# Performance work log

Hardware: AMD Instinct MI355X
Metric: run time of the kernel (lower is better)

Reference implementation:

```python
import jax, jax.numpy as jnp
import numpy as np

B, L, D, H, DH, FF = 4, 1024, 1024, 16, 64, 4096
EPS = 1e-5


def _layer_norm(x, g, b):
    m = jnp.mean(x, -1, keepdims=True)
    v = jnp.mean((x - m) ** 2, -1, keepdims=True)
    return (x - m) * jax.lax.rsqrt(v + EPS) * g + b


def setup_inputs() -> dict:
    key = jax.random.key(0)
    ks = jax.random.split(key, 20)
    s = 0.02  # param init scale
    return {
        "x": jax.random.normal(ks[0], (B, L, D), jnp.float32),
        "adj_mask_matrix": jax.random.uniform(ks[1], (B * H, L, L), jnp.float32),
        "com_mask_matrix": jax.random.uniform(ks[2], (B * H, L, L), jnp.float32),
        "lattice_rel": jax.random.normal(ks[3], (2, 1, 1, DH), jnp.float32),
        "Wq": jax.random.normal(ks[4], (D, D), jnp.float32) * s,
        "bq": jnp.zeros((D,), jnp.float32),
        "Wk": jax.random.normal(ks[5], (D, D), jnp.float32) * s,
        "bk": jnp.zeros((D,), jnp.float32),
        "Wv": jax.random.normal(ks[6], (D, D), jnp.float32) * s,
        "bv": jnp.zeros((D,), jnp.float32),
        "Wo": jax.random.normal(ks[7], (D, D), jnp.float32) * s,
        "bo": jnp.zeros((D,), jnp.float32),
        "ln1_scale": jnp.ones((D,), jnp.float32),
        "ln1_bias": jnp.zeros((D,), jnp.float32),
        "W1": jax.random.normal(ks[8], (D, FF), jnp.float32) * s,
        "b1": jnp.zeros((FF,), jnp.float32),
        "W2": jax.random.normal(ks[9], (FF, D), jnp.float32) * s,
        "b2": jnp.zeros((D,), jnp.float32),
        "ln2_scale": jnp.ones((D,), jnp.float32),
        "ln2_bias": jnp.zeros((D,), jnp.float32),
    }


def reference(x, adj_mask_matrix, com_mask_matrix, lattice_rel,
              Wq, bq, Wk, bk, Wv, bv, Wo, bo, ln1_scale, ln1_bias,
              W1, b1, W2, b2, ln2_scale, ln2_bias):
    Bsz, Ln, Dm = x.shape
    # QKV projections; flat reshape [B,L,H*dh] -> [B*H,L,dh] matches torch .view
    Q = (x @ Wq + bq).reshape(Bsz * H, Ln, DH)
    K = (x @ Wk + bk).reshape(Bsz * H, Ln, DH)
    V = (x @ Wv + bv).reshape(Bsz * H, Ln, DH)
    scale = DH ** (-0.5)
    adj_rel = lattice_rel[0]  # [1,1,dh] broadcasts over (B*H, L)
    com_rel = lattice_rel[1]
    att_adj = jnp.einsum('bqd,bkd->bqk', Q + adj_rel, K + adj_rel) * scale
    att_com = jnp.einsum('bqd,bkd->bqk', Q + com_rel, K + com_rel) * scale
    # post-softmax multiplicative masking, then sum of the two attention maps
    mask_att = (jax.nn.softmax(att_adj, axis=-1) * adj_mask_matrix
                + jax.nn.softmax(att_com, axis=-1) * com_mask_matrix)
    context = jnp.matmul(mask_att, V).reshape(Bsz, Ln, H * DH)
    out = _layer_norm(context @ Wo + bo + x, ln1_scale, ln1_bias)
    ff = jax.nn.relu(out @ W1 + b1) @ W2 + b2
    return _layer_norm(ff + out, ln2_scale, ln2_bias)
```

## Files before the change

kernel.cpp:

```cpp
#include <hip/hip_runtime.h>
#include <hip/hip_bf16.h>

typedef __attribute__((ext_vector_type(8))) short s16x8;
typedef __attribute__((ext_vector_type(4))) float f32x4;
typedef unsigned short u16;
typedef unsigned int u32;

__device__ __forceinline__ u16 f2b(float f) {
    u32 u = __float_as_uint(f);
    u32 r = (u + 0x7fffu + ((u >> 16) & 1u)) >> 16;
    return (u16)r;
}
__device__ __forceinline__ float b2f(u16 b) {
    return __uint_as_float(((u32)b) << 16);
}

#define MFMA16(a, b, c) __builtin_amdgcn_mfma_f32_16x16x32_bf16(a, b, c, 0, 0, 0)
#define GLDS(gp, lp)                                                              \
    __builtin_amdgcn_global_load_lds((const __attribute__((address_space(1))) void*)(gp), \
                                     (__attribute__((address_space(3))) void*)(lp), 16, 0, 0)

__global__ void k_f2b(const float* __restrict__ in, u16* __restrict__ out, int n4) {
    int i = blockIdx.x * 256 + threadIdx.x;
    if (i >= n4) return;
    float4 v = ((const float4*)in)[i];
    ushort4 o;
    o.x = f2b(v.x); o.y = f2b(v.y); o.z = f2b(v.z); o.w = f2b(v.w);
    ((ushort4*)out)[i] = o;
}

__global__ void k_wtrans(const float* __restrict__ W, u16* __restrict__ Wt, int K, int N) {
    __shared__ float t[32][33];
    int bx = blockIdx.x * 32, by = blockIdx.y * 32;
    int tx = threadIdx.x, ty = threadIdx.y;
    for (int i = 0; i < 32; i += 8)
        t[ty + i][tx] = W[(size_t)(by + ty + i) * N + bx + tx];
    __syncthreads();
    for (int i = 0; i < 32; i += 8)
        Wt[(size_t)(bx + ty + i) * K + by + tx] = f2b(t[tx][ty + i]);
}

__global__ __launch_bounds__(256) void gemm_qkv(const u16* __restrict__ A, const u16* __restrict__ Bt,
                                                const float* __restrict__ bq, const float* __restrict__ bk,
                                                const float* __restrict__ bv,
                                                u16* __restrict__ Qb, u16* __restrict__ Kb,
                                                u16* __restrict__ Vt) {
    __shared__ __align__(16) short lA[128 * 64];
    __shared__ __align__(16) short lB[128 * 64];
    const int tid = threadIdx.x, lane = tid & 63, w = tid >> 6;
    const int l15 = lane & 15, lg = lane >> 4;
    const int wr = w >> 1, wc = w & 1;
    const int m0 = blockIdx.y * 128, n0 = blockIdx.x * 128;
    const int KK = 1024;
    f32x4 acc[4][4] = {};

    for (int k0 = 0; k0 < KK; k0 += 64) {
        #pragma unroll
        for (int i = 0; i < 4; i++) {
            int chunk = w * 4 + i;
            int arow = m0 + chunk * 8 + (lane >> 3);
            GLDS(A + (size_t)arow * KK + k0 + (lane & 7) * 8, (short*)lA + chunk * 512);
            int brow = n0 + chunk * 8 + (lane >> 3);
            GLDS(Bt + (size_t)brow * KK + k0 + (lane & 7) * 8, (short*)lB + chunk * 512);
        }
        __syncthreads();
        #pragma unroll
        for (int ks = 0; ks < 2; ks++) {
            s16x8 af[4], bfr[4];
            #pragma unroll
            for (int m = 0; m < 4; m++)
                af[m] = *(const s16x8*)&lA[(wr * 64 + m * 16 + l15) * 64 + ks * 32 + lg * 8];
            #pragma unroll
            for (int n = 0; n < 4; n++)
                bfr[n] = *(const s16x8*)&lB[(wc * 64 + n * 16 + l15) * 64 + ks * 32 + lg * 8];
            #pragma unroll
            for (int m = 0; m < 4; m++)
                #pragma unroll
                for (int n = 0; n < 4; n++)
                    acc[m][n] = MFMA16(af[m], bfr[n], acc[m][n]);
        }
        __syncthreads();
    }
    const int rbase = m0 + wr * 64, cbase = n0 + wc * 64;
    const int seg = cbase >> 10;
    #pragma unroll
    for (int m = 0; m < 4; m++)
        #pragma unroll
        for (int n = 0; n < 4; n++) {
            int col = cbase + n * 16 + l15;
            int c1 = col & 1023, d = col & 63;
            int row0 = rbase + m * 16 + lg * 4;
            if (seg == 0) {
                float bb = bq[c1];
                #pragma unroll
                for (int r = 0; r < 4; r++)
                    Qb[(size_t)(row0 + r) * 1024 + c1] = f2b(acc[m][n][r] + bb);
            } else if (seg == 1) {
                float bb = bk[c1];
                #pragma unroll
                for (int r = 0; r < 4; r++)
                    Kb[(size_t)(row0 + r) * 1024 + c1] = f2b(acc[m][n][r] + bb);
            } else {
                float bb = bv[c1];
                #pragma unroll
                for (int r = 0; r < 4; r++) {
                    int row = row0 + r;
                    size_t o = (size_t)(row >> 6) * 65536 + (size_t)d * 1024 + (row & 63) * 16 + (c1 >> 6);
                    Vt[o] = f2b(acc[m][n][r] + bb);
                }
            }
        }
}

template <int EPI>
__global__ __launch_bounds__(256) void gemm_bt(const u16* __restrict__ A, const u16* __restrict__ Bt,
                                               void* __restrict__ Cv, int M, int N, int K,
                                               const float* __restrict__ bias) {
    __shared__ __align__(16) short lA[128 * 64];
    __shared__ __align__(16) short lB[128 * 64];
    const int tid = threadIdx.x, lane = tid & 63, w = tid >> 6;
    const int l15 = lane & 15, lg = lane >> 4;
    const int wr = w >> 1, wc = w & 1;
    const int m0 = blockIdx.y * 128, n0 = blockIdx.x * 128;
    f32x4 acc[4][4] = {};

    for (int k0 = 0; k0 < K; k0 += 64) {
        #pragma unroll
        for (int i = 0; i < 4; i++) {
            int chunk = w * 4 + i;
            int arow = m0 + chunk * 8 + (lane >> 3);
            GLDS(A + (size_t)arow * K + k0 + (lane & 7) * 8, (short*)lA + chunk * 512);
            int brow = n0 + chunk * 8 + (lane >> 3);
            GLDS(Bt + (size_t)brow * K + k0 + (lane & 7) * 8, (short*)lB + chunk * 512);
        }
        __syncthreads();
        #pragma unroll
        for (int ks = 0; ks < 2; ks++) {
            s16x8 af[4], bfr[4];
            #pragma unroll
            for (int m = 0; m < 4; m++)
                af[m] = *(const s16x8*)&lA[(wr * 64 + m * 16 + l15) * 64 + ks * 32 + lg * 8];
            #pragma unroll
            for (int n = 0; n < 4; n++)
                bfr[n] = *(const s16x8*)&lB[(wc * 64 + n * 16 + l15) * 64 + ks * 32 + lg * 8];
            #pragma unroll
            for (int m = 0; m < 4; m++)
                #pragma unroll
                for (int n = 0; n < 4; n++)
                    acc[m][n] = MFMA16(af[m], bfr[n], acc[m][n]);
        }
        __syncthreads();
    }
    const int rbase = m0 + wr * 64, cbase = n0 + wc * 64;
    #pragma unroll
    for (int m = 0; m < 4; m++)
        #pragma unroll
        for (int n = 0; n < 4; n++) {
            int col = cbase + n * 16 + l15;
            int row0 = rbase + m * 16 + lg * 4;
            u16* C = (u16*)Cv;
            float bv = bias[col];
            #pragma unroll
            for (int r = 0; r < 4; r++)
                C[(size_t)(row0 + r) * N + col] = f2b(fmaxf(acc[m][n][r] + bv, 0.f));
        }
}

__global__ __launch_bounds__(256) void gemm_bt64(const u16* __restrict__ A, const u16* __restrict__ Bt,
                                                 float* __restrict__ C, int M, int N, int K) {
    __shared__ __align__(16) short lA[128 * 64];
    __shared__ __align__(16) short lB[64 * 64];
    const int tid = threadIdx.x, lane = tid & 63, w = tid >> 6;
    const int l15 = lane & 15, lg = lane >> 4;
    const int m0 = blockIdx.y * 128, n0 = blockIdx.x * 64;
    f32x4 acc[2][4] = {};

    for (int k0 = 0; k0 < K; k0 += 64) {
        #pragma unroll
        for (int i = 0; i < 4; i++) {
            int chunk = w * 4 + i;
            int arow = m0 + chunk * 8 + (lane >> 3);
            GLDS(A + (size_t)arow * K + k0 + (lane & 7) * 8, (short*)lA + chunk * 512);
        }
        #pragma unroll
        for (int i = 0; i < 2; i++) {
            int chunk = w * 2 + i;
            int brow = n0 + chunk * 8 + (lane >> 3);
            GLDS(Bt + (size_t)brow * K + k0 + (lane & 7) * 8, (short*)lB + chunk * 512);
        }
        __syncthreads();
        #pragma unroll
        for (int ks = 0; ks < 2; ks++) {
            s16x8 af[2], bfr[4];
            #pragma unroll
            for (int m = 0; m < 2; m++)
                af[m] = *(const s16x8*)&lA[(w * 32 + m * 16 + l15) * 64 + ks * 32 + lg * 8];
            #pragma unroll
            for (int n = 0; n < 4; n++)
                bfr[n] = *(const s16x8*)&lB[(n * 16 + l15) * 64 + ks * 32 + lg * 8];
            #pragma unroll
            for (int m = 0; m < 2; m++)
                #pragma unroll
                for (int n = 0; n < 4; n++)
                    acc[m][n] = MFMA16(af[m], bfr[n], acc[m][n]);
        }
        __syncthreads();
    }
    #pragma unroll
    for (int m = 0; m < 2; m++)
        #pragma unroll
        for (int n = 0; n < 4; n++) {
            int col = n0 + n * 16 + l15;
            int row0 = m0 + w * 32 + m * 16 + lg * 4;
            #pragma unroll
            for (int r = 0; r < 4; r++)
                C[(size_t)(row0 + r) * N + col] = acc[m][n][r];
        }
}

__global__ void k_fvec(const u16* __restrict__ Kb, const float* __restrict__ rel,
                       float* __restrict__ fa, float* __restrict__ fc) {
    __shared__ float rs[128];
    const int g = blockIdx.x, tid = threadIdx.x;
    if (tid < 128) rs[tid] = rel[tid];
    __syncthreads();
    for (int k = tid; k < 1024; k += 256) {
        const u16* kr = Kb + (size_t)g * 65536 + (size_t)k * 64;
        float sa = 0.f, sc = 0.f;
        #pragma unroll
        for (int j = 0; j < 8; j++) {
            s16x8 v = *(const s16x8*)(kr + j * 8);
            #pragma unroll
            for (int e = 0; e < 8; e++) {
                float kv = b2f((u16)v[e]);
                sa += kv * rs[j * 8 + e];
                sc += kv * rs[64 + j * 8 + e];
            }
        }
        fa[g * 1024 + k] = __expf(sa * 0.125f);
        fc[g * 1024 + k] = __expf(sc * 0.125f);
    }
}

__global__ __launch_bounds__(256, 2) void k_qke0(const u16* __restrict__ Qb, const u16* __restrict__ Kb,
                                                 const float* __restrict__ fa, const float* __restrict__ fc,
                                                 u16* __restrict__ E0,
                                                 float* __restrict__ la_, float* __restrict__ lc_) {
    const int bid = blockIdx.x;
    const int xcd = bid & 7, j = bid >> 3;
    const int g = xcd * 8 + (j & 7), qt = j >> 3;
    const int tid = threadIdx.x, lane = tid & 63, w = tid >> 6;
    const int l15 = lane & 15, lg = lane >> 4;
    __shared__ __align__(16) float lE[4][16][68];

    const int q0 = qt * 64 + w * 16;
    const size_t gQ = (size_t)g * 65536;
    const float scale = 0.125f;

    s16x8 qf[2];
    #pragma unroll
    for (int ks = 0; ks < 2; ks++)
        qf[ks] = *(const s16x8*)(Qb + gQ + (size_t)(q0 + l15) * 64 + ks * 32 + lg * 8);

    float la[4] = {0.f, 0.f, 0.f, 0.f}, lc[4] = {0.f, 0.f, 0.f, 0.f};
    const int srow = lane >> 2, sjj = lane & 3;

    #pragma unroll 1
    for (int it = 0; it < 16; it++) {
        const int kb = it * 64;
        f32x4 sa[4] = {};
        s16x8 kf[8];
        #pragma unroll
        for (int ks = 0; ks < 2; ks++)
            #pragma unroll
            for (int n = 0; n < 4; n++)
                kf[ks * 4 + n] = *(const s16x8*)(Kb + gQ + (size_t)(kb + n * 16 + l15) * 64 + ks * 32 + lg * 8);
        #pragma unroll
        for (int ks = 0; ks < 2; ks++)
            #pragma unroll
            for (int n = 0; n < 4; n++)
                sa[n] = MFMA16(qf[ks], kf[ks * 4 + n], sa[n]);
        #pragma unroll
        for (int n = 0; n < 4; n++) {
            float fav = fa[g * 1024 + kb + n * 16 + l15];
            float fcv = fc[g * 1024 + kb + n * 16 + l15];
            #pragma unroll
            for (int r = 0; r < 4; r++) {
                float er = b2f(f2b(__expf(sa[n][r] * scale)));
                la[r] += er * fav;
                lc[r] += er * fcv;
                lE[w][lg * 4 + r][n * 16 + l15] = er;
            }
        }
        {
            const float* lp = &lE[w][srow][sjj * 16];
            uint4 p0, p1;
            p0.x = (u32)f2b(lp[0]) | ((u32)f2b(lp[1]) << 16);
            p0.y = (u32)f2b(lp[2]) | ((u32)f2b(lp[3]) << 16);
            p0.z = (u32)f2b(lp[4]) | ((u32)f2b(lp[5]) << 16);
            p0.w = (u32)f2b(lp[6]) | ((u32)f2b(lp[7]) << 16);
            p1.x = (u32)f2b(lp[8]) | ((u32)f2b(lp[9]) << 16);
            p1.y = (u32)f2b(lp[10]) | ((u32)f2b(lp[11]) << 16);
            p1.z = (u32)f2b(lp[12]) | ((u32)f2b(lp[13]) << 16);
            p1.w = (u32)f2b(lp[14]) | ((u32)f2b(lp[15]) << 16);
            u16* ep = E0 + (size_t)g * 1048576 + (size_t)(q0 + srow) * 1024 + kb + sjj * 16;
            *(uint4*)ep = p0;
            *(uint4*)(ep + 8) = p1;
        }
    }
    #pragma unroll
    for (int r = 0; r < 4; r++)
        #pragma unroll
        for (int m = 8; m >= 1; m >>= 1) {
            la[r] += __shfl_xor(la[r], m);
            lc[r] += __shfl_xor(lc[r], m);
        }
    if (l15 == 0) {
        #pragma unroll
        for (int r = 0; r < 4; r++) {
            la_[g * 1024 + q0 + lg * 4 + r] = la[r];
            lc_[g * 1024 + q0 + lg * 4 + r] = lc[r];
        }
    }
}

__global__ void k_pmul(const u16* __restrict__ E0, const float* __restrict__ Ma, const float* __restrict__ Mc,
                       const float* __restrict__ fa, const float* __restrict__ fc,
                       const float* __restrict__ la, const float* __restrict__ lc,
                       u16* __restrict__ P) {
    int idx = blockIdx.x * 256 + threadIdx.x;
    int g = idx >> 17;
    int q = (idx >> 7) & 1023;
    int k0 = (idx & 127) * 8;
    size_t base = (size_t)idx * 8;
    s16x8 e = *(const s16x8*)(E0 + base);
    float4 m0 = *(const float4*)(Ma + base), m1 = *(const float4*)(Ma + base + 4);
    float4 n0 = *(const float4*)(Mc + base), n1 = *(const float4*)(Mc + base + 4);
    int fi = g * 1024 + k0;
    float4 a0 = *(const float4*)(fa + fi), a1 = *(const float4*)(fa + fi + 4);
    float4 c0 = *(const float4*)(fc + fi), c1 = *(const float4*)(fc + fi + 4);
    float ila = 1.f / la[g * 1024 + q];
    float ilc = 1.f / lc[g * 1024 + q];
    uint4 o;
    o.x = (u32)f2b(b2f((u16)e[0]) * (a0.x * m0.x * ila + c0.x * n0.x * ilc)) |
          ((u32)f2b(b2f((u16)e[1]) * (a0.y * m0.y * ila + c0.y * n0.y * ilc)) << 16);
    o.y = (u32)f2b(b2f((u16)e[2]) * (a0.z * m0.z * ila + c0.z * n0.z * ilc)) |
          ((u32)f2b(b2f((u16)e[3]) * (a0.w * m0.w * ila + c0.w * n0.w * ilc)) << 16);
    o.z = (u32)f2b(b2f((u16)e[4]) * (a1.x * m1.x * ila + c1.x * n1.x * ilc)) |
          ((u32)f2b(b2f((u16)e[5]) * (a1.y * m1.y * ila + c1.y * n1.y * ilc)) << 16);
    o.w = (u32)f2b(b2f((u16)e[6]) * (a1.z * m1.z * ila + c1.z * n1.z * ilc)) |
          ((u32)f2b(b2f((u16)e[7]) * (a1.w * m1.w * ila + c1.w * n1.w * ilc)) << 16);
    *(uint4*)(P + base) = o;
}

__global__ __launch_bounds__(256) void gemm_pv(const u16* __restrict__ P, const u16* __restrict__ Vt,
                                               u16* __restrict__ ctx) {
    __shared__ __align__(16) short lA[128 * 64];
    __shared__ __align__(16) short lB[64 * 64];
    const int tid = threadIdx.x, lane = tid & 63, w = tid >> 6;
    const int l15 = lane & 15, lg = lane >> 4;
    const int g = blockIdx.y, m0 = blockIdx.x * 128;
    const u16* A = P + (size_t)g * 1048576;
    const u16* Bt = Vt + (size_t)g * 65536;
    f32x4 acc[2][4] = {};

    for (int k0 = 0; k0 < 1024; k0 += 64) {
        #pragma unroll
        for (int i = 0; i < 4; i++) {
            int chunk = w * 4 + i;
            int arow = m0 + chunk * 8 + (lane >> 3);
            GLDS(A + (size_t)arow * 1024 + k0 + (lane & 7) * 8, (short*)lA + chunk * 512);
        }
        #pragma unroll
        for (int i = 0; i < 2; i++) {
            int chunk = w * 2 + i;
            int brow = chunk * 8 + (lane >> 3);
            GLDS(Bt + (size_t)brow * 1024 + k0 + (lane & 7) * 8, (short*)lB + chunk * 512);
        }
        __syncthreads();
        #pragma unroll
        for (int ks = 0; ks < 2; ks++) {
            s16x8 af[2], bfr[4];
            #pragma unroll
            for (int m = 0; m < 2; m++)
                af[m] = *(const s16x8*)&lA[(w * 32 + m * 16 + l15) * 64 + ks * 32 + lg * 8];
            #pragma unroll
            for (int n = 0; n < 4; n++)
                bfr[n] = *(const s16x8*)&lB[(n * 16 + l15) * 64 + ks * 32 + lg * 8];
            #pragma unroll
            for (int m = 0; m < 2; m++)
                #pragma unroll
                for (int n = 0; n < 4; n++)
                    acc[m][n] = MFMA16(af[m], bfr[n], acc[m][n]);
        }
        __syncthreads();
    }
    #pragma unroll
    for (int m = 0; m < 2; m++)
        #pragma unroll
        for (int n = 0; n < 4; n++) {
            int col = n * 16 + l15;
            int row0 = m0 + w * 32 + m * 16 + lg * 4;
            #pragma unroll
            for (int r = 0; r < 4; r++)
                ctx[(size_t)g * 65536 + (size_t)(row0 + r) * 64 + col] = f2b(acc[m][n][r]);
        }
}

__global__ __launch_bounds__(256) void k_ln(const float* __restrict__ a, const float* __restrict__ bias,
                                            const float* __restrict__ resid, const float* __restrict__ gamma,
                                            const float* __restrict__ beta, float* __restrict__ out,
                                            u16* __restrict__ outb) {
    const int row = blockIdx.x, tid = threadIdx.x;
    const size_t base = (size_t)row * 1024 + tid * 4;
    float4 av = *(const float4*)(a + base);
    float4 rv = *(const float4*)(resid + base);
    float4 bv = *(const float4*)(bias + tid * 4);
    float t0 = av.x + rv.x + bv.x, t1 = av.y + rv.y + bv.y;
    float t2 = av.z + rv.z + bv.z, t3 = av.w + rv.w + bv.w;
    __shared__ float red[4];
    float s = t0 + t1 + t2 + t3;
    #pragma unroll
    for (int m = 32; m >= 1; m >>= 1) s += __shfl_xor(s, m);
    int w = tid >> 6;
    if ((tid & 63) == 0) red[w] = s;
    __syncthreads();
    float mean = (red[0] + red[1] + red[2] + red[3]) * (1.f / 1024.f);
    float d0 = t0 - mean, d1 = t1 - mean, d2 = t2 - mean, d3 = t3 - mean;
    float q = d0 * d0 + d1 * d1 + d2 * d2 + d3 * d3;
    __syncthreads();
    #pragma unroll
    for (int m = 32; m >= 1; m >>= 1) q += __shfl_xor(q, m);
    if ((tid & 63) == 0) red[w] = q;
    __syncthreads();
    float var = (red[0] + red[1] + red[2] + red[3]) * (1.f / 1024.f);
    float rs = rsqrtf(var + 1e-5f);
    float4 gv = *(const float4*)(gamma + tid * 4);
    float4 bev = *(const float4*)(beta + tid * 4);
    float o0 = d0 * rs * gv.x + bev.x, o1 = d1 * rs * gv.y + bev.y;
    float o2 = d2 * rs * gv.z + bev.z, o3 = d3 * rs * gv.w + bev.w;
    *(float4*)(out + base) = make_float4(o0, o1, o2, o3);
    if (outb) {
        ushort4 ob;
        ob.x = f2b(o0); ob.y = f2b(o1); ob.z = f2b(o2); ob.w = f2b(o3);
        *(ushort4*)(outb + base) = ob;
    }
}

extern "C" void kernel_launch(void* const* d_in, const int* in_sizes, int n_in,
                              void* d_out, int out_size, void* d_ws, size_t ws_size,
                              hipStream_t stream) {
    const float* x    = (const float*)d_in[0];
    const float* adjm = (const float*)d_in[1];
    const float* comm = (const float*)d_in[2];
    const float* rel  = (const float*)d_in[3];
    const float* Wq   = (const float*)d_in[4];
    const float* bq   = (const float*)d_in[5];
    const float* Wk   = (const float*)d_in[6];
    const float* bk   = (const float*)d_in[7];
    const float* Wv   = (const float*)d_in[8];
    const float* bv   = (const float*)d_in[9];
    const float* Wo   = (const float*)d_in[10];
    const float* bo   = (const float*)d_in[11];
    const float* g1   = (const float*)d_in[12];
    const float* be1  = (const float*)d_in[13];
    const float* W1   = (const float*)d_in[14];
    const float* b1   = (const float*)d_in[15];
    const float* W2   = (const float*)d_in[16];
    const float* b2   = (const float*)d_in[17];
    const float* g2   = (const float*)d_in[18];
    const float* be2  = (const float*)d_in[19];
    float* out = (float*)d_out;

    char* ws = (char*)d_ws;
    const size_t MB = 1048576;
    u16*   xb    = (u16*)(ws + 0 * MB);
    u16*   Wqkvt = (u16*)(ws + 8 * MB);
    u16*   Wot   = (u16*)(ws + 14 * MB);
    u16*   W1t   = (u16*)(ws + 16 * MB);
    u16*   W2t   = (u16*)(ws + 24 * MB);
    u16*   Qb    = (u16*)(ws + 32 * MB);
    u16*   Kb    = (u16*)(ws + 40 * MB);
    u16*   Vtb   = (u16*)(ws + 48 * MB);
    float* faB   = (float*)(ws + 56 * MB);
    float* fcB   = (float*)(ws + 56 * MB + 262144);
    float* laB   = (float*)(ws + 56 * MB + 524288);
    float* lcB   = (float*)(ws + 56 * MB + 786432);
    u16*   E0b   = (u16*)(ws + 57 * MB);
    u16*   Pb    = (u16*)(ws + 185 * MB);
    u16*   ctx   = (u16*)(ws + 313 * MB);
    float* ctxWo = (float*)(ws + 57 * MB);
    float* out1  = (float*)(ws + 73 * MB);
    u16*   out1b = (u16*)(ws + 89 * MB);
    u16*   rb    = (u16*)(ws + 97 * MB);
    float* ff2   = (float*)(ws + 129 * MB);

    dim3 tb(32, 8);
    k_f2b<<<4096, 256, 0, stream>>>(x, xb, 1048576);
    k_wtrans<<<dim3(32, 32), tb, 0, stream>>>(Wq, Wqkvt, 1024, 1024);
    k_wtrans<<<dim3(32, 32), tb, 0, stream>>>(Wk, Wqkvt + 1024 * 1024, 1024, 1024);
    k_wtrans<<<dim3(32, 32), tb, 0, stream>>>(Wv, Wqkvt + 2 * 1024 * 1024, 1024, 1024);
    k_wtrans<<<dim3(32, 32), tb, 0, stream>>>(Wo, Wot, 1024, 1024);
    k_wtrans<<<dim3(128, 32), tb, 0, stream>>>(W1, W1t, 1024, 4096);
    k_wtrans<<<dim3(32, 128), tb, 0, stream>>>(W2, W2t, 4096, 1024);
    gemm_qkv<<<dim3(24, 32), 256, 0, stream>>>(xb, Wqkvt, bq, bk, bv, Qb, Kb, Vtb);
    k_fvec<<<64, 256, 0, stream>>>(Kb, rel, faB, fcB);
    k_qke0<<<1024, 256, 0, stream>>>(Qb, Kb, faB, fcB, E0b, laB, lcB);
    k_pmul<<<32768, 256, 0, stream>>>(E0b, adjm, comm, faB, fcB, laB, lcB, Pb);
    gemm_pv<<<dim3(8, 64), 256, 0, stream>>>(Pb, Vtb, ctx);
    gemm_bt64<<<dim3(16, 32), 256, 0, stream>>>(ctx, Wot, ctxWo, 4096, 1024, 1024);
    k_ln<<<4096, 256, 0, stream>>>(ctxWo, bo, x, g1, be1, out1, out1b);
    gemm_bt<1><<<dim3(32, 32), 256, 0, stream>>>(out1b, W1t, rb, 4096, 4096, 1024, b1);
    gemm_bt64<<<dim3(16, 32), 256, 0, stream>>>(rb, W2t, ff2, 4096, 1024, 4096);
    k_ln<<<4096, 256, 0, stream>>>(ff2, b2, out1, g2, be2, out, nullptr);
}
```

Baseline: 562.5 us.

## Fuse post-softmax mask multiply into the PV matmul kernel

Replaces the separate elementwise kernel that built the masked probability matrix P with a fused kernel that streams the masks, normalizers and exponentials tile by tile into LDS and feeds bf16 P directly to MFMA against V. This removes writing and rereading the full bf16 P tensor in global memory. In exchange the fused kernel uses large LDS buffers, which limits occupancy, and has no load/compute double buffering. Workspace offsets are compacted.

```diff
diff --git a/kernel.cpp b/kernel.cpp
--- a/kernel.cpp
+++ b/kernel.cpp
@@ -324,87 +324,94 @@
     }
 }
 
-__global__ void k_pmul(const u16* __restrict__ E0, const float* __restrict__ Ma, const float* __restrict__ Mc,
-                       const float* __restrict__ fa, const float* __restrict__ fc,
-                       const float* __restrict__ la, const float* __restrict__ lc,
-                       u16* __restrict__ P) {
-    int idx = blockIdx.x * 256 + threadIdx.x;
-    int g = idx >> 17;
-    int q = (idx >> 7) & 1023;
-    int k0 = (idx & 127) * 8;
-    size_t base = (size_t)idx * 8;
-    s16x8 e = *(const s16x8*)(E0 + base);
-    float4 m0 = *(const float4*)(Ma + base), m1 = *(const float4*)(Ma + base + 4);
-    float4 n0 = *(const float4*)(Mc + base), n1 = *(const float4*)(Mc + base + 4);
-    int fi = g * 1024 + k0;
-    float4 a0 = *(const float4*)(fa + fi), a1 = *(const float4*)(fa + fi + 4);
-    float4 c0 = *(const float4*)(fc + fi), c1 = *(const float4*)(fc + fi + 4);
-    float ila = 1.f / la[g * 1024 + q];
-    float ilc = 1.f / lc[g * 1024 + q];
-    uint4 o;
-    o.x = (u32)f2b(b2f((u16)e[0]) * (a0.x * m0.x * ila + c0.x * n0.x * ilc)) |
-          ((u32)f2b(b2f((u16)e[1]) * (a0.y * m0.y * ila + c0.y * n0.y * ilc)) << 16);
-    o.y = (u32)f2b(b2f((u16)e[2]) * (a0.z * m0.z * ila + c0.z * n0.z * ilc)) |
-          ((u32)f2b(b2f((u16)e[3]) * (a0.w * m0.w * ila + c0.w * n0.w * ilc)) << 16);
-    o.z = (u32)f2b(b2f((u16)e[4]) * (a1.x * m1.x * ila + c1.x * n1.x * ilc)) |
-          ((u32)f2b(b2f((u16)e[5]) * (a1.y * m1.y * ila + c1.y * n1.y * ilc)) << 16);
-    o.w = (u32)f2b(b2f((u16)e[6]) * (a1.z * m1.z * ila + c1.z * n1.z * ilc)) |
-          ((u32)f2b(b2f((u16)e[7]) * (a1.w * m1.w * ila + c1.w * n1.w * ilc)) << 16);
-    *(uint4*)(P + base) = o;
-}
-
-__global__ __launch_bounds__(256) void gemm_pv(const u16* __restrict__ P, const u16* __restrict__ Vt,
-                                               u16* __restrict__ ctx) {
-    __shared__ __align__(16) short lA[128 * 64];
-    __shared__ __align__(16) short lB[64 * 64];
+__global__ __launch_bounds__(256) void gemm_pvf(const u16* __restrict__ E0, const u16* __restrict__ Vt,
+                                                const float* __restrict__ Ma_g, const float* __restrict__ Mc_g,
+                                                const float* __restrict__ fa, const float* __restrict__ fc,
+                                                const float* __restrict__ la, const float* __restrict__ lc,
+                                                u16* __restrict__ ctx) {
+    __shared__ __align__(16) float bufMa[64 * 64];
+    __shared__ __align__(16) float bufMc[64 * 64];
+    __shared__ __align__(16) short bufP[64 * 68];
+    __shared__ __align__(16) short bufV[64 * 68];
+    __shared__ __align__(16) float lfa[1024];
+    __shared__ __align__(16) float lfc[1024];
+
+    const int bid = blockIdx.x;
+    const int xcd = bid & 7, j = bid >> 3;
+    const int g = xcd * 8 + (j & 7), qt = j >> 3;
     const int tid = threadIdx.x, lane = tid & 63, w = tid >> 6;
     const int l15 = lane & 15, lg = lane >> 4;
-    const int g = blockIdx.y, m0 = blockIdx.x * 128;
-    const u16* A = P + (size_t)g * 1048576;
-    const u16* Bt = Vt + (size_t)g * 65536;
-    f32x4 acc[2][4] = {};
-
-    for (int k0 = 0; k0 < 1024; k0 += 64) {
-        #pragma unroll
-        for (int i = 0; i < 4; i++) {
-            int chunk = w * 4 + i;
-            int arow = m0 + chunk * 8 + (lane >> 3);
-            GLDS(A + (size_t)arow * 1024 + k0 + (lane & 7) * 8, (short*)lA + chunk * 512);
-        }
-        #pragma unroll
-        for (int i = 0; i < 2; i++) {
-            int chunk = w * 2 + i;
-            int brow = chunk * 8 + (lane >> 3);
-            GLDS(Bt + (size_t)brow * 1024 + k0 + (lane & 7) * 8, (short*)lB + chunk * 512);
+    const int q0 = qt * 64;
+    const size_t gE = (size_t)g * 1048576;
+    const size_t gV = (size_t)g * 65536;
+
+    GLDS(fa + g * 1024 + w * 256 + (lane & 63) * 4, lfa + w * 256);
+    GLDS(fc + g * 1024 + w * 256 + (lane & 63) * 4, lfc + w * 256);
+    const int pr = tid >> 2, pc = (tid & 3) * 16;
+    const float ila = 1.f / la[g * 1024 + q0 + pr];
+    const float ilc = 1.f / lc[g * 1024 + q0 + pr];
+    const int vd = tid >> 2, vc = (tid & 3) * 16;
+
+    f32x4 acc[4] = {};
+    __syncthreads();
+
+    #pragma unroll 1
+    for (int it = 0; it < 16; it++) {
+        const int kb = it * 64;
+        #pragma unroll
+        for (int o = 0; o < 4; o++) {
+            int op = w * 4 + o;
+            int row = op * 4 + (lane >> 4);
+            int ch = lane & 15;
+            GLDS(Ma_g + (size_t)g * 1048576 + (size_t)(q0 + row) * 1024 + kb + ch * 4, bufMa + op * 256);
+            GLDS(Mc_g + (size_t)g * 1048576 + (size_t)(q0 + row) * 1024 + kb + ch * 4, bufMc + op * 256);
+        }
+        s16x8 v0 = *(const s16x8*)(Vt + gV + (size_t)vd * 1024 + kb + vc);
+        s16x8 v1 = *(const s16x8*)(Vt + gV + (size_t)vd * 1024 + kb + vc + 8);
+        s16x8 e0 = *(const s16x8*)(E0 + gE + (size_t)(q0 + pr) * 1024 + kb + pc);
+        s16x8 e1 = *(const s16x8*)(E0 + gE + (size_t)(q0 + pr) * 1024 + kb + pc + 8);
+        *(s16x8*)&bufV[vd * 68 + vc] = v0;
+        *(s16x8*)&bufV[vd * 68 + vc + 8] = v1;
+        __syncthreads();
+        {
+            const float* map = &bufMa[pr * 64 + pc];
+            const float* mcp = &bufMc[pr * 64 + pc];
+            const float* fap = &lfa[kb + pc];
+            const float* fcp = &lfc[kb + pc];
+            union { s16x8 v; u16 u[8]; } o0, o1;
+            #pragma unroll
+            for (int e = 0; e < 8; e++) {
+                float t = fap[e] * map[e] * ila + fcp[e] * mcp[e] * ilc;
+                o0.u[e] = f2b(b2f((u16)e0[e]) * t);
+            }
+            #pragma unroll
+            for (int e = 0; e < 8; e++) {
+                float t = fap[8 + e] * map[8 + e] * ila + fcp[8 + e] * mcp[8 + e] * ilc;
+                o1.u[e] = f2b(b2f((u16)e1[e]) * t);
+            }
+            *(s16x8*)&bufP[pr * 68 + pc] = o0.v;
+            *(s16x8*)&bufP[pr * 68 + pc + 8] = o1.v;
         }
         __syncthreads();
         #pragma unroll
         for (int ks = 0; ks < 2; ks++) {
-            s16x8 af[2], bfr[4];
-            #pragma unroll
-            for (int m = 0; m < 2; m++)
-                af[m] = *(const s16x8*)&lA[(w * 32 + m * 16 + l15) * 64 + ks * 32 + lg * 8];
-            #pragma unroll
-            for (int n = 0; n < 4; n++)
-                bfr[n] = *(const s16x8*)&lB[(n * 16 + l15) * 64 + ks * 32 + lg * 8];
-            #pragma unroll
-            for (int m = 0; m < 2; m++)
-                #pragma unroll
-                for (int n = 0; n < 4; n++)
-                    acc[m][n] = MFMA16(af[m], bfr[n], acc[m][n]);
-        }
-        __syncthreads();
-    }
-    #pragma unroll
-    for (int m = 0; m < 2; m++)
-        #pragma unroll
-        for (int n = 0; n < 4; n++) {
-            int col = n * 16 + l15;
-            int row0 = m0 + w * 32 + m * 16 + lg * 4;
-            #pragma unroll
-            for (int r = 0; r < 4; r++)
-                ctx[(size_t)g * 65536 + (size_t)(row0 + r) * 64 + col] = f2b(acc[m][n][r]);
-        }
+            s16x8 af = *(const s16x8*)&bufP[(w * 16 + l15) * 68 + ks * 32 + lg * 8];
+            #pragma unroll
+            for (int n = 0; n < 4; n++) {
+                s16x8 bfr = *(const s16x8*)&bufV[(n * 16 + l15) * 68 + ks * 32 + lg * 8];
+                acc[n] = MFMA16(af, bfr, acc[n]);
+            }
+        }
+        __syncthreads();
+    }
+    #pragma unroll
+    for (int n = 0; n < 4; n++) {
+        int col = n * 16 + l15;
+        int row0 = q0 + w * 16 + lg * 4;
+        #pragma unroll
+        for (int r = 0; r < 4; r++)
+            ctx[gV + (size_t)(row0 + r) * 64 + col] = f2b(acc[n][r]);
+    }
 }
 
 __global__ __launch_bounds__(256) void k_ln(const float* __restrict__ a, const float* __restrict__ bias,
@@ -487,13 +494,12 @@
     float* laB   = (float*)(ws + 56 * MB + 524288);
     float* lcB   = (float*)(ws + 56 * MB + 786432);
     u16*   E0b   = (u16*)(ws + 57 * MB);
-    u16*   Pb    = (u16*)(ws + 185 * MB);
-    u16*   ctx   = (u16*)(ws + 313 * MB);
-    float* ctxWo = (float*)(ws + 57 * MB);
-    float* out1  = (float*)(ws + 73 * MB);
-    u16*   out1b = (u16*)(ws + 89 * MB);
-    u16*   rb    = (u16*)(ws + 97 * MB);
-    float* ff2   = (float*)(ws + 129 * MB);
+    u16*   ctx   = (u16*)(ws + 185 * MB);
+    float* ctxWo = (float*)(ws + 193 * MB);
+    float* out1  = (float*)(ws + 209 * MB);
+    u16*   out1b = (u16*)(ws + 225 * MB);
+    u16*   rb    = (u16*)(ws + 233 * MB);
+    float* ff2   = (float*)(ws + 265 * MB);
 
     dim3 tb(32, 8);
     k_f2b<<<4096, 256, 0, stream>>>(x, xb, 1048576);
@@ -506,8 +512,7 @@
     gemm_qkv<<<dim3(24, 32), 256, 0, stream>>>(xb, Wqkvt, bq, bk, bv, Qb, Kb, Vtb);
     k_fvec<<<64, 256, 0, stream>>>(Kb, rel, faB, fcB);
     k_qke0<<<1024, 256, 0, stream>>>(Qb, Kb, faB, fcB, E0b, laB, lcB);
-    k_pmul<<<32768, 256, 0, stream>>>(E0b, adjm, comm, faB, fcB, laB, lcB, Pb);
-    gemm_pv<<<dim3(8, 64), 256, 0, stream>>>(Pb, Vtb, ctx);
+    gemm_pvf<<<1024, 256, 0, stream>>>(E0b, Vtb, adjm, comm, faB, fcB, laB, lcB, ctx);
     gemm_bt64<<<dim3(16, 32), 256, 0, stream>>>(ctx, Wot, ctxWo, 4096, 1024, 1024);
     k_ln<<<4096, 256, 0, stream>>>(ctxWo, bo, x, g1, be1, out1, out1b);
     gemm_bt<1><<<dim3(32, 32), 256, 0, stream>>>(out1b, W1t, rb, 4096, 4096, 1024, b1);
```

Measured after the change: 548.2 us, median of 2. -2.5%, faster.
